# Kernel tuning notes

Hardware: AMD Instinct MI355X
Metric: run time of the kernel (lower is better)

Reference implementation:

```python
import jax, jax.numpy as jnp
import numpy as np

B = 8192
INPUT_DIM = 64   # history length / freq_dim
OUTPUT_DIM = 16
TEXT_DIM = 1024
TEXT_AIM = 128
H = 128          # lstm hidden_size (2 layers)


def _lin(key, out_d, in_d):
    k1, k2 = jax.random.split(key)
    s = 1.0 / np.sqrt(in_d)
    w = jax.random.uniform(k1, (out_d, in_d), jnp.float32, -s, s)
    b = jax.random.uniform(k2, (out_d,), jnp.float32, -s, s)
    return w, b


def setup_inputs() -> dict:
    key = jax.random.key(0)
    ks = jax.random.split(key, 16)
    inp = {}
    inp["data"] = jax.random.normal(ks[0], (B, INPUT_DIM), jnp.float32)
    inp["text_feature"] = jax.random.normal(ks[1], (B, TEXT_DIM), jnp.float32)
    # CrossAttention(text_aim_dim=128, freq_dim=input_dim=64)
    inp["q_w"], inp["q_b"] = _lin(ks[2], INPUT_DIM, INPUT_DIM)
    inp["k_w"], inp["k_b"] = _lin(ks[3], INPUT_DIM, TEXT_AIM)
    inp["v_w"], inp["v_b"] = _lin(ks[4], INPUT_DIM, TEXT_AIM)
    # text_proj: 1024 -> 256 -> 128
    inp["tp1_w"], inp["tp1_b"] = _lin(ks[5], 256, TEXT_DIM)
    inp["tp2_w"], inp["tp2_b"] = _lin(ks[6], TEXT_AIM, 256)
    # gate: 64 -> 128 -> 64
    inp["g1_w"], inp["g1_b"] = _lin(ks[7], 128, INPUT_DIM)
    inp["g2_w"], inp["g2_b"] = _lin(ks[8], INPUT_DIM, 128)
    # 2-layer LSTM, input size 1 (PyTorch i,f,g,o gate order)
    inp["w_ih0"], inp["b_ih0"] = _lin(ks[9], 4 * H, 1)
    inp["w_hh0"], inp["b_hh0"] = _lin(ks[10], 4 * H, H)
    inp["w_ih1"], inp["b_ih1"] = _lin(ks[11], 4 * H, H)
    inp["w_hh1"], inp["b_hh1"] = _lin(ks[12], 4 * H, H)
    # fc head: H -> H -> 1
    inp["fc1_w"], inp["fc1_b"] = _lin(ks[13], H, H)
    inp["fc2_w"], inp["fc2_b"] = _lin(ks[14], 1, H)
    return inp


def _cell(x, h, c, w_ih, w_hh, b_ih, b_hh):
    g = x @ w_ih.T + h @ w_hh.T + (b_ih + b_hh)
    i, f, gg, o = jnp.split(g, 4, axis=-1)
    c = jax.nn.sigmoid(f) * c + jax.nn.sigmoid(i) * jnp.tanh(gg)
    h = jax.nn.sigmoid(o) * jnp.tanh(c)
    return h, c


def _forward(data, text_feature, q_w, q_b, k_w, k_b, v_w, v_b,
             tp1_w, tp1_b, tp2_w, tp2_b, g1_w, g1_b, g2_w, g2_b,
             w_ih0, b_ih0, w_hh0, b_hh0, w_ih1, b_ih1, w_hh1, b_hh1,
             fc1_w, fc1_b, fc2_w, fc2_b):
    Bn = data.shape[0]
    z = jnp.zeros((Bn, H), data.dtype)
    # --- warmup pass over the full sequence (seq-major xs: (T, B, 1)) ---
    xs = data.T[:, :, None]

    def warm(carry, x_t):
        h0, c0, h1, c1 = carry
        h0, c0 = _cell(x_t, h0, c0, w_ih0, w_hh0, b_ih0, b_hh0)
        h1, c1 = _cell(h0, h1, c1, w_ih1, w_hh1, b_ih1, b_hh1)
        return (h0, c0, h1, c1), None

    (h0, c0, h1, c1), _ = jax.lax.scan(warm, (z, z, z, z), xs)

    def dec(carry, _):
        h0, c0, h1, c1, x_t = carry
        h0, c0 = _cell(x_t, h0, c0, w_ih0, w_hh0, b_ih0, b_hh0)
        h1, c1 = _cell(h0, h1, c1, w_ih1, w_hh1, b_ih1, b_hh1)
        hmid = jax.nn.leaky_relu(h1 @ fc1_w.T + fc1_b)
        pred = hmid @ fc2_w.T + fc2_b  # (B, 1)
        return (h0, c0, h1, c1, pred), pred

    (_, _, _, _, _), preds = jax.lax.scan(dec, (h0, c0, h1, c1, data[:, -1:]), None, length=OUTPUT_DIM)
    result = preds[:, :, 0].T  # (B, OUTPUT_DIM)

    # --- text-enhance branch: FFT features + cross-attention gating ---
    X = jnp.fft.rfft(data)                       # (B, 33)
    amp = jnp.abs(X)
    phase = jnp.angle(X)
    fftres = jnp.concatenate([amp, phase[:, 1:]], axis=1)  # (B, 65)
    dc, feat = fftres[:, :1], fftres[:, 1:]                # (B,1), (B,64)

    tp = jax.nn.leaky_relu(text_feature @ tp1_w.T + tp1_b) @ tp2_w.T + tp2_b  # (B, 128)
    Q = feat @ q_w.T + q_b
    K = tp @ k_w.T + k_b
    V = tp @ v_w.T + v_b
    adj = jax.nn.softmax(Q * K, axis=-1) * V  # (B, 64)

    gate = jax.nn.sigmoid(jax.nn.leaky_relu(adj @ g1_w.T + g1_b) @ g2_w.T + g2_b)  # (B, 64)

    full = jnp.concatenate([jnp.zeros_like(dc), adj], axis=1)  # (B, 65)
    n_freq = INPUT_DIM // 2
    amp2 = full[:, :n_freq + 1]                                 # (B, 33)
    ph2 = jnp.concatenate([jnp.zeros_like(dc), full[:, n_freq + 1:]], axis=1)  # (B, 33)
    Xr = jax.lax.complex(amp2 * jnp.cos(ph2), amp2 * jnp.sin(ph2))
    recon = jnp.fft.irfft(Xr, n=INPUT_DIM)  # (B, 64)

    g16 = gate[:, :OUTPUT_DIM]
    return g16 * result + (1.0 - g16) * recon[:, :OUTPUT_DIM]


def reference(data, text_feature, q_w, q_b, k_w, k_b, v_w, v_b,
              tp1_w, tp1_b, tp2_w, tp2_b, g1_w, g1_b, g2_w, g2_b,
              w_ih0, b_ih0, w_hh0, b_hh0, w_ih1, b_ih1, w_hh1, b_hh1,
              fc1_w, fc1_b, fc2_w, fc2_b):
    return _forward(data, text_feature, q_w, q_b, k_w, k_b, v_w, v_b,
                    tp1_w, tp1_b, tp2_w, tp2_b, g1_w, g1_b, g2_w, g2_b,
                    w_ih0, b_ih0, w_hh0, b_hh0, w_ih1, b_ih1, w_hh1, b_hh1,
                    fc1_w, fc1_b, fc2_w, fc2_b)
```

## Files before the change

### kernel.cpp

```cpp
#include <hip/hip_runtime.h>
#include <hip/hip_fp16.h>
#include <math.h>

typedef _Float16 half8 __attribute__((ext_vector_type(8)));
typedef float f32x4 __attribute__((ext_vector_type(4)));

#define W0F 0.09817477042468103f

#if __has_builtin(__builtin_amdgcn_exp2f)
#define EXP2F __builtin_amdgcn_exp2f
#else
#define EXP2F exp2f
#endif
#if __has_builtin(__builtin_amdgcn_rcpf)
#define RCPF __builtin_amdgcn_rcpf
#else
#define RCPF(x) (1.f/(x))
#endif

__device__ __forceinline__ float sigf(float x){
  return RCPF(1.f + EXP2F(-1.442695041f*x));
}
__device__ __forceinline__ float tanh_fast(float x){
  float t = EXP2F(2.885390082f*x);
  return 1.f - 2.f*RCPF(t + 1.f);
}
__device__ __forceinline__ float lrelu(float x){ return (x>0.f)? x : 0.01f*x; }

__device__ __forceinline__ uint32_t packhl(float x){
  __half h = __float2half(x);
  __half l = __float2half(x - __half2float(h));
  return (uint32_t)__half_as_ushort(h) | ((uint32_t)__half_as_ushort(l) << 16);
}

__device__ __forceinline__ void unpackA(const uint4 d0, const uint4 d1, half8& hi, half8& lo){
  union { half8 h; uint32_t u[4]; } H, L;
  H.u[0] = (d0.x & 0xffffu) | (d0.y << 16);
  H.u[1] = (d0.z & 0xffffu) | (d0.w << 16);
  H.u[2] = (d1.x & 0xffffu) | (d1.y << 16);
  H.u[3] = (d1.z & 0xffffu) | (d1.w << 16);
  L.u[0] = (d0.x >> 16) | (d0.y & 0xffff0000u);
  L.u[1] = (d0.z >> 16) | (d0.w & 0xffff0000u);
  L.u[2] = (d1.x >> 16) | (d1.y & 0xffff0000u);
  L.u[3] = (d1.z >> 16) | (d1.w & 0xffff0000u);
  hi = H.h; lo = L.h;
}

__device__ __forceinline__ f32x4 mfma2(half8 ah, half8 al, half8 bh, f32x4 c){
  c = __builtin_amdgcn_mfma_f32_16x16x32_f16(ah, bh, c, 0,0,0);
  c = __builtin_amdgcn_mfma_f32_16x16x32_f16(al, bh, c, 0,0,0);
  return c;
}

__global__ __launch_bounds__(256) void convert_w(
    const float* __restrict__ w_hh0, const float* __restrict__ w_ih1,
    const float* __restrict__ w_hh1, const float* __restrict__ fc1_w,
    const float* __restrict__ tp1_w, __half* __restrict__ wsH)
{
  int c = blockIdx.x*256 + threadIdx.x;
  const float* src; size_t dhi, dlo; int n, k, K;
  if (c < 24576){
    int m = c >> 13; int q = c & 8191;
    src = (m==0)? w_hh0 : ((m==1)? w_ih1 : w_hh1); K = 128;
    dhi = (size_t)m*131072 + (size_t)q*8; dlo = dhi + 65536;
    int tile = q >> 8, ks = (q >> 6) & 3, lane = q & 63;
    n = tile*16 + (lane & 15); k = ks*32 + (lane >> 4)*8;
  } else if (c < 26624){
    int q = c - 24576; src = fc1_w; K = 128;
    dhi = 393216 + (size_t)q*8; dlo = 409600 + (size_t)q*8;
    int tile = q >> 8, ks = (q >> 6) & 3, lane = q & 63;
    n = tile*16 + (lane & 15); k = ks*32 + (lane >> 4)*8;
  } else {
    int q = c - 26624; src = tp1_w; K = 1024;
    dhi = 425984 + (size_t)q*8; dlo = 688128 + (size_t)q*8;
    int tile = q >> 11, ks = (q >> 6) & 31, lane = q & 63;
    n = tile*16 + (lane & 15); k = ks*32 + (lane >> 4)*8;
  }
  float4 a = *(const float4*)(src + (size_t)n*K + k);
  float4 b = *(const float4*)(src + (size_t)n*K + k + 4);
  float vv[8] = {a.x,a.y,a.z,a.w,b.x,b.y,b.z,b.w};
  union { uint4 u; unsigned short s[8]; } HI, LO;
  #pragma unroll
  for (int j = 0; j < 8; ++j){
    __half hh = __float2half(vv[j]);
    __half ll = __float2half(vv[j] - __half2float(hh));
    HI.s[j] = __half_as_ushort(hh);
    LO.s[j] = __half_as_ushort(ll);
  }
  *(uint4*)(wsH + dhi) = HI.u;
  *(uint4*)(wsH + dlo) = LO.u;
}

__global__ __attribute__((amdgpu_flat_work_group_size(512,512), amdgpu_waves_per_eu(2,2)))
void mkty_main(
    const float* __restrict__ data, const float* __restrict__ text_feature,
    const float* __restrict__ q_w, const float* __restrict__ q_b,
    const float* __restrict__ k_w, const float* __restrict__ k_b,
    const float* __restrict__ v_w, const float* __restrict__ v_b,
    const float* __restrict__ tp1_b,
    const float* __restrict__ tp2_w, const float* __restrict__ tp2_b,
    const float* __restrict__ g1_w, const float* __restrict__ g1_b,
    const float* __restrict__ g2_w, const float* __restrict__ g2_b,
    const float* __restrict__ w_ih0, const float* __restrict__ b_ih0,
    const float* __restrict__ b_hh0,
    const float* __restrict__ b_ih1, const float* __restrict__ b_hh1,
    const float* __restrict__ fc1_b,
    const float* __restrict__ fc2_w, const float* __restrict__ fc2_b,
    const __half* __restrict__ wsH, float* __restrict__ out)
{
  __shared__ float s_x[32][64];
  __shared__ float s_gate[32][16];
  __shared__ float s_rec[32][16];
  __shared__ float s_res[32][16];
  __shared__ float s_pred[32];
  __shared__ float ctab[64], stab[64];
  __shared__ __align__(16) unsigned char POOL[84992];

  const int tid = threadIdx.x;
  const int w = tid >> 6, l = tid & 63;
  const int lm = l & 15, lq = l >> 4;
  const int s0blk = blockIdx.x * 32;

  { int s = tid >> 4, j = (tid*4) & 63;
    *(float4*)&s_x[s][j] = *(const float4*)(data + (size_t)(s0blk+s)*64 + j); }
  if (tid < 64){ float sv,cv; sincosf((float)tid*W0F,&sv,&cv);
    stab[tid] = (tid==32)?0.f:sv; ctab[tid]=cv; }
  __syncthreads();

  {
    float* h256 = (float*)POOL;
    uint32_t* tfp = (uint32_t*)(POOL + 33792);
    const half8* T1h = (const half8*)(wsH + 425984);
    const int t0 = 2*w;
    f32x4 acc[2][2];
    #pragma unroll
    for (int mt=0; mt<2; ++mt)
      #pragma unroll
      for (int nt=0; nt<2; ++nt){ f32x4 z = {0.f,0.f,0.f,0.f}; acc[mt][nt] = z; }
    for (int kc = 0; kc < 1024; kc += 64){
      __syncthreads();
      { int s = tid >> 4, j0 = (tid & 15)*4;
        float4 v = *(const float4*)(text_feature + (size_t)(s0blk+s)*1024 + kc + j0);
        uint4 p; p.x = packhl(v.x); p.y = packhl(v.y); p.z = packhl(v.z); p.w = packhl(v.w);
        *(uint4*)&tfp[s*68 + j0] = p; }
      __syncthreads();
      #pragma unroll
      for (int ks = 0; ks < 2; ++ks){
        half8 Ah[2], Al[2];
        #pragma unroll
        for (int mt = 0; mt < 2; ++mt){
          const uint32_t* pp = &tfp[(mt*16+lm)*68 + ks*32 + lq*8];
          unpackA(*(const uint4*)pp, *(const uint4*)(pp+4), Ah[mt], Al[mt]);
        }
        int ksg = (kc >> 5) + ks;
        #pragma unroll
        for (int nt = 0; nt < 2; ++nt){
          int ci = ((t0+nt)*32 + ksg)*64 + l;
          half8 bh = T1h[ci];
          #pragma unroll
          for (int mt = 0; mt < 2; ++mt)
            acc[mt][nt] = mfma2(Ah[mt],Al[mt],bh,acc[mt][nt]);
        }
      }
    }
    #pragma unroll
    for (int nt = 0; nt < 2; ++nt){
      int n = (t0+nt)*16 + lm;
      float bb = tp1_b[n];
      #pragma unroll
      for (int mt = 0; mt < 2; ++mt)
        #pragma unroll
        for (int r = 0; r < 4; ++r)
          h256[(mt*16 + lq*4 + r)*260 + n] = lrelu(acc[mt][nt][r] + bb);
    }
  }
  __syncthreads();

  {
    const float* h256 = (const float*)POOL;
    int o = tid & 127, soct = tid >> 7, ss = soct*8;
    float acc8[8];
    #pragma unroll
    for (int i=0;i<8;++i) acc8[i]=0.f;
    const float4* w2r = (const float4*)(tp2_w + o*256);
    #pragma unroll 4
    for (int k4 = 0; k4 < 64; ++k4){
      float4 w4 = w2r[k4];
      #pragma unroll
      for (int i = 0; i < 8; ++i){
        float4 hv = *(const float4*)&h256[(ss+i)*260 + k4*4];
        acc8[i] += w4.x*hv.x; acc8[i] += w4.y*hv.y;
        acc8[i] += w4.z*hv.z; acc8[i] += w4.w*hv.w;
      }
    }
    __syncthreads();
    float* tpT = (float*)(POOL + 33792);
    float bb = tp2_b[o];
    #pragma unroll
    for (int i=0;i<8;++i) tpT[(ss+i)*128 + o] = acc8[i] + bb;
  }
  __syncthreads();

  {
    float* featT = (float*)POOL;
    #pragma unroll
    for (int i = 0; i < 2; ++i){
      int task = tid + 512*i;
      int s = task >> 5;
      int k = (task & 31) + 1;
      float re = 0.f, im = 0.f;
      #pragma unroll 8
      for (int n = 0; n < 64; ++n){
        float d = s_x[s][n];
        int m = (k*n) & 63;
        re += d*ctab[m]; im -= d*stab[m];
      }
      if (k == 32) im = 0.f;
      featT[(k-1)*32 + s] = sqrtf(re*re + im*im);
      featT[(31+k)*32 + s] = atan2f(im, re);
    }
  }
  __syncthreads();

  {
    const float* featT = (const float*)POOL;
    const float* tpT = (const float*)(POOL + 33792);
    float* QK = (float*)(POOL + 8192);
    float* V  = (float*)(POOL + 16384);
    #pragma unroll
    for (int i = 0; i < 4; ++i){
      int task = tid + 512*i;
      int s = task >> 6, o = task & 63;
      float q = q_b[o];
      const float* qwr = q_w + o*64;
      #pragma unroll 4
      for (int k = 0; k < 64; ++k) q += qwr[k]*featT[k*32 + s];
      float kk = k_b[o], vv = v_b[o];
      const float* kwr = k_w + o*128;
      const float* vwr = v_w + o*128;
      const float* tps = tpT + s*128;
      #pragma unroll 4
      for (int k = 0; k < 128; ++k){ kk += kwr[k]*tps[k]; vv += vwr[k]*tps[k]; }
      QK[s*64+o] = q*kk; V[s*64+o] = vv;
    }
  }
  __syncthreads();

  if (tid < 32){
    float* QK = (float*)(POOL + 8192);
    const float* V = (const float*)(POOL + 16384);
    float mx = -1e30f;
    for (int o = 0; o < 64; ++o) mx = fmaxf(mx, QK[tid*64+o]);
    float sum = 0.f;
    for (int o = 0; o < 64; ++o){ float e = expf(QK[tid*64+o]-mx); QK[tid*64+o] = e; sum += e; }
    float inv = 1.f/sum;
    for (int o = 0; o < 64; ++o) QK[tid*64+o] *= inv*V[tid*64+o];
  }
  __syncthreads();

  {
    const float* ADJ = (const float*)(POOL + 8192);
    float* midT = (float*)(POOL + 33792);
    int j = tid & 127, soct = tid >> 7, ss = soct*8;
    float accm[8];
    float bb = g1_b[j];
    #pragma unroll
    for (int i=0;i<8;++i) accm[i]=bb;
    const float* wr = g1_w + j*64;
    #pragma unroll 4
    for (int k = 0; k < 64; ++k){
      float ww = wr[k];
      #pragma unroll
      for (int i=0;i<8;++i) accm[i] += ww*ADJ[(ss+i)*64 + k];
    }
    #pragma unroll
    for (int i=0;i<8;++i) midT[(ss+i)*128 + j] = lrelu(accm[i]);
  }
  __syncthreads();

  {
    int s = tid >> 4, o = tid & 15;
    const float* midT = (const float*)(POOL + 33792);
    const float* ADJ = (const float*)(POOL + 8192);
    float acc = g2_b[o];
    const float* wr = g2_w + o*128;
    #pragma unroll 4
    for (int k = 0; k < 128; ++k) acc += wr[k]*midT[s*128 + k];
    float gate = sigf(acc);
    float sum = 0.f;
    float a32 = ADJ[s*64+31], p32 = ADJ[s*64+63];
    #pragma unroll
    for (int k = 1; k < 32; ++k){
      float amp = ADJ[s*64 + k-1];
      float ph  = ADJ[s*64 + 31+k];
      int m = (k*o) & 63;
      sum += amp*cosf(ph + (float)m*W0F);
    }
    float parity = (o&1)? -1.f : 1.f;
    s_gate[s][o] = gate;
    s_rec[s][o] = (2.f*sum + parity*a32*cosf(p32))*(1.f/64.f);
  }
  __syncthreads();

  { uint32_t* hz = (uint32_t*)POOL;
    for (int i = tid; i < 13568; i += 512) hz[i] = 0; }
  if (tid < 32) s_pred[tid] = s_x[tid][63];

  const int u = 16*w + lm;
  float bias0[4], wx0[4], bias1[4];
  #pragma unroll
  for (int T = 0; T < 4; ++T){
    int n = T*128 + u;
    bias0[T] = b_ih0[n] + b_hh0[n];
    wx0[T]   = w_ih0[n];
    bias1[T] = b_ih1[n] + b_hh1[n];
  }
  const float fb = fc1_b[u];
  const float wcol = fc2_w[u];
  const float fb2 = fc2_b[0];
  const half8* WH0h = (const half8*)(wsH);
  const half8* WI1h = (const half8*)(wsH + 131072);
  const half8* WH1h = (const half8*)(wsH + 262144);
  const half8* F1h  = (const half8*)(wsH + 393216);
  __half* h0h = (__half*)(POOL);
  __half* h1h = (__half*)(POOL + 8704);
  float*  c0s = (float*)(POOL + 17408);
  float*  c1s = (float*)(POOL + 35840);
  float*  fc2p = (float*)(POOL + 54272);
  const int cbase = w*256 + l;

  half8 wh0[16], wi1[16], wh1[16];
  #pragma unroll
  for (int q = 0; q < 16; ++q){
    int nt = q >> 2, ks = q & 3;
    int ci = nt*2048 + ks*64 + cbase;
    wh0[q] = WH0h[ci];
    wi1[q] = WI1h[ci];
    wh1[q] = WH1h[ci];
  }
  #pragma unroll
  for (int q = 0; q < 16; ++q)
    asm volatile("" : "+v"(wh0[q]), "+v"(wi1[q]), "+v"(wh1[q]));
  __syncthreads();

  for (int t = 0; t < 80; ++t){
    float xv[2][4];
    #pragma unroll
    for (int mt = 0; mt < 2; ++mt)
      #pragma unroll
      for (int r = 0; r < 4; ++r){
        int m = mt*16 + lq*4 + r;
        xv[mt][r] = (t < 64) ? s_x[m][t] : s_pred[m];
      }
    f32x4 acc0[2][4];
    #pragma unroll
    for (int nt = 0; nt < 4; ++nt)
      #pragma unroll
      for (int mt = 0; mt < 2; ++mt){
        f32x4 a;
        #pragma unroll
        for (int r = 0; r < 4; ++r) a[r] = bias0[nt] + wx0[nt]*xv[mt][r];
        acc0[mt][nt] = a;
      }
    #pragma unroll
    for (int ks = 0; ks < 4; ++ks){
      half8 Ah[2];
      #pragma unroll
      for (int mt = 0; mt < 2; ++mt)
        Ah[mt] = *(const half8*)&h0h[(mt*16+lm)*136 + ks*32 + lq*8];
      #pragma unroll
      for (int nt = 0; nt < 4; ++nt)
        #pragma unroll
        for (int mt = 0; mt < 2; ++mt)
          acc0[mt][nt] = __builtin_amdgcn_mfma_f32_16x16x32_f16(Ah[mt], wh0[nt*4+ks], acc0[mt][nt], 0,0,0);
    }
    __syncthreads();
    #pragma unroll
    for (int mt = 0; mt < 2; ++mt)
      #pragma unroll
      for (int r = 0; r < 4; ++r){
        int cix = tid*9 + mt*4 + r;
        float gi = acc0[mt][0][r], gf = acc0[mt][1][r];
        float gg = acc0[mt][2][r], go = acc0[mt][3][r];
        float c = sigf(gf)*c0s[cix] + sigf(gi)*tanh_fast(gg);
        float h = sigf(go)*tanh_fast(c);
        c0s[cix] = c;
        h0h[(mt*16 + lq*4 + r)*136 + u] = __float2half(h);
      }
    __syncthreads();
    f32x4 acc1[2][4];
    #pragma unroll
    for (int nt = 0; nt < 4; ++nt)
      #pragma unroll
      for (int mt = 0; mt < 2; ++mt){
        f32x4 a; float bb = bias1[nt];
        a[0]=bb; a[1]=bb; a[2]=bb; a[3]=bb;
        acc1[mt][nt] = a;
      }
    #pragma unroll
    for (int ks = 0; ks < 4; ++ks){
      half8 Ah[2];
      #pragma unroll
      for (int mt = 0; mt < 2; ++mt)
        Ah[mt] = *(const half8*)&h0h[(mt*16+lm)*136 + ks*32 + lq*8];
      #pragma unroll
      for (int nt = 0; nt < 4; ++nt)
        #pragma unroll
        for (int mt = 0; mt < 2; ++mt)
          acc1[mt][nt] = __builtin_amdgcn_mfma_f32_16x16x32_f16(Ah[mt], wi1[nt*4+ks], acc1[mt][nt], 0,0,0);
    }
    #pragma unroll
    for (int ks = 0; ks < 4; ++ks){
      half8 Ah[2];
      #pragma unroll
      for (int mt = 0; mt < 2; ++mt)
        Ah[mt] = *(const half8*)&h1h[(mt*16+lm)*136 + ks*32 + lq*8];
      #pragma unroll
      for (int nt = 0; nt < 4; ++nt)
        #pragma unroll
        for (int mt = 0; mt < 2; ++mt)
          acc1[mt][nt] = __builtin_amdgcn_mfma_f32_16x16x32_f16(Ah[mt], wh1[nt*4+ks], acc1[mt][nt], 0,0,0);
    }
    __syncthreads();
    #pragma unroll
    for (int mt = 0; mt < 2; ++mt)
      #pragma unroll
      for (int r = 0; r < 4; ++r){
        int cix = tid*9 + mt*4 + r;
        float gi = acc1[mt][0][r], gf = acc1[mt][1][r];
        float gg = acc1[mt][2][r], go = acc1[mt][3][r];
        float c = sigf(gf)*c1s[cix] + sigf(gi)*tanh_fast(gg);
        float h = sigf(go)*tanh_fast(c);
        c1s[cix] = c;
        h1h[(mt*16 + lq*4 + r)*136 + u] = __float2half(h);
      }
    __syncthreads();

    if (t >= 64){
      f32x4 fa[2];
      #pragma unroll
      for (int mt = 0; mt < 2; ++mt){ f32x4 a; a[0]=fb;a[1]=fb;a[2]=fb;a[3]=fb; fa[mt]=a; }
      #pragma unroll
      for (int ks = 0; ks < 4; ++ks){
        half8 Ah[2];
        #pragma unroll
        for (int mt = 0; mt < 2; ++mt)
          Ah[mt] = *(const half8*)&h1h[(mt*16+lm)*136 + ks*32 + lq*8];
        int ci = (w*4 + ks)*64 + l;
        half8 bh = F1h[ci];
        #pragma unroll
        for (int mt = 0; mt < 2; ++mt)
          fa[mt] = __builtin_amdgcn_mfma_f32_16x16x32_f16(Ah[mt], bh, fa[mt], 0,0,0);
      }
      float pr[2][4];
      #pragma unroll
      for (int mt = 0; mt < 2; ++mt)
        #pragma unroll
        for (int r = 0; r < 4; ++r){
          float p = lrelu(fa[mt][r]) * wcol;
          p += __shfl_xor(p, 1, 16);
          p += __shfl_xor(p, 2, 16);
          p += __shfl_xor(p, 4, 16);
          p += __shfl_xor(p, 8, 16);
          pr[mt][r] = p;
        }
      if (lm == 0){
        #pragma unroll
        for (int mt = 0; mt < 2; ++mt)
          #pragma unroll
          for (int r = 0; r < 4; ++r)
            fc2p[(mt*16 + lq*4 + r)*8 + w] = pr[mt][r];
      }
      __syncthreads();
      if (tid < 32){
        float s = fb2;
        #pragma unroll
        for (int j = 0; j < 8; ++j) s += fc2p[tid*8 + j];
        s_pred[tid] = s;
        s_res[tid][t-64] = s;
      }
      __syncthreads();
    }
  }

  {
    int s = tid >> 4, d = tid & 15;
    float g = s_gate[s][d];
    out[(size_t)blockIdx.x*512 + tid] = g*s_res[s][d] + (1.f - g)*s_rec[s][d];
  }
}

extern "C" void kernel_launch(void* const* d_in, const int* in_sizes, int n_in,
                              void* d_out, int out_size, void* d_ws, size_t ws_size,
                              hipStream_t stream){
  const float* data =(const float*)d_in[0];
  const float* tf   =(const float*)d_in[1];
  const float* q_w  =(const float*)d_in[2];  const float* q_b  =(const float*)d_in[3];
  const float* k_w  =(const float*)d_in[4];  const float* k_b  =(const float*)d_in[5];
  const float* v_w  =(const float*)d_in[6];  const float* v_b  =(const float*)d_in[7];
  const float* tp1_w=(const float*)d_in[8];  const float* tp1_b=(const float*)d_in[9];
  const float* tp2_w=(const float*)d_in[10]; const float* tp2_b=(const float*)d_in[11];
  const float* g1_w =(const float*)d_in[12]; const float* g1_b =(const float*)d_in[13];
  const float* g2_w =(const float*)d_in[14]; const float* g2_b =(const float*)d_in[15];
  const float* w_ih0=(const float*)d_in[16]; const float* b_ih0=(const float*)d_in[17];
  const float* w_hh0=(const float*)d_in[18]; const float* b_hh0=(const float*)d_in[19];
  const float* w_ih1=(const float*)d_in[20]; const float* b_ih1=(const float*)d_in[21];
  const float* w_hh1=(const float*)d_in[22]; const float* b_hh1=(const float*)d_in[23];
  const float* fc1_w=(const float*)d_in[24]; const float* fc1_b=(const float*)d_in[25];
  const float* fc2_w=(const float*)d_in[26]; const float* fc2_b=(const float*)d_in[27];
  float* out=(float*)d_out;
  __half* wsH = (__half*)d_ws;

  convert_w<<<232,256,0,stream>>>(w_hh0, w_ih1, w_hh1, fc1_w, tp1_w, wsH);
  mkty_main<<<256,512,0,stream>>>(data, tf, q_w,q_b, k_w,k_b, v_w,v_b,
                                  tp1_b, tp2_w,tp2_b, g1_w,g1_b, g2_w,g2_b,
                                  w_ih0,b_ih0,b_hh0, b_ih1,b_hh1,
                                  fc1_b, fc2_w,fc2_b, wsH, out);
}
```

Measured before the change: 834.2 us.

## Double-buffer LSTM hidden states in LDS to drop two barriers per step

```diff
diff --git a/kernel.cpp b/kernel.cpp
--- a/kernel.cpp
+++ b/kernel.cpp
@@ -303,7 +303,7 @@
   __syncthreads();
 
   { uint32_t* hz = (uint32_t*)POOL;
-    for (int i = tid; i < 13568; i += 512) hz[i] = 0; }
+    for (int i = tid; i < 17920; i += 512) hz[i] = 0; }
   if (tid < 32) s_pred[tid] = s_x[tid][63];
 
   const int u = 16*w + lm;
@@ -322,28 +322,41 @@
   const half8* WI1h = (const half8*)(wsH + 131072);
   const half8* WH1h = (const half8*)(wsH + 262144);
   const half8* F1h  = (const half8*)(wsH + 393216);
-  __half* h0h = (__half*)(POOL);
-  __half* h1h = (__half*)(POOL + 8704);
-  float*  c0s = (float*)(POOL + 17408);
-  float*  c1s = (float*)(POOL + 35840);
-  float*  fc2p = (float*)(POOL + 54272);
+  __half* h0base = (__half*)(POOL);
+  __half* h1base = (__half*)(POOL + 17408);
+  float*  c0s = (float*)(POOL + 34816);
+  float*  c1s = (float*)(POOL + 53248);
+  float*  fc2p = (float*)(POOL + 71680);
   const int cbase = w*256 + l;
 
-  half8 wh0[16], wi1[16], wh1[16];
+  half8 wh0[16], wi1[16], wh1c[8];
   #pragma unroll
   for (int q = 0; q < 16; ++q){
     int nt = q >> 2, ks = q & 3;
     int ci = nt*2048 + ks*64 + cbase;
     wh0[q] = WH0h[ci];
     wi1[q] = WI1h[ci];
-    wh1[q] = WH1h[ci];
+  }
+  #pragma unroll
+  for (int q = 0; q < 8; ++q){
+    int nt = q >> 1, ks = q & 1;
+    wh1c[q] = WH1h[nt*2048 + ks*64 + cbase];
   }
   #pragma unroll
   for (int q = 0; q < 16; ++q)
-    asm volatile("" : "+v"(wh0[q]), "+v"(wi1[q]), "+v"(wh1[q]));
+    asm volatile("" : "+v"(wh0[q]), "+v"(wi1[q]));
+  #pragma unroll
+  for (int q = 0; q < 8; ++q)
+    asm volatile("" : "+v"(wh1c[q]));
   __syncthreads();
 
   for (int t = 0; t < 80; ++t){
+    const int cur = t & 1;
+    __half* h0r = h0base + cur*4352;
+    __half* h0w = h0base + (cur^1)*4352;
+    __half* h1r = h1base + cur*4352;
+    __half* h1w = h1base + (cur^1)*4352;
+
     float xv[2][4];
     #pragma unroll
     for (int mt = 0; mt < 2; ++mt)
@@ -367,14 +380,13 @@
       half8 Ah[2];
       #pragma unroll
       for (int mt = 0; mt < 2; ++mt)
-        Ah[mt] = *(const half8*)&h0h[(mt*16+lm)*136 + ks*32 + lq*8];
+        Ah[mt] = *(const half8*)&h0r[(mt*16+lm)*136 + ks*32 + lq*8];
       #pragma unroll
       for (int nt = 0; nt < 4; ++nt)
         #pragma unroll
         for (int mt = 0; mt < 2; ++mt)
           acc0[mt][nt] = __builtin_amdgcn_mfma_f32_16x16x32_f16(Ah[mt], wh0[nt*4+ks], acc0[mt][nt], 0,0,0);
     }
-    __syncthreads();
     #pragma unroll
     for (int mt = 0; mt < 2; ++mt)
       #pragma unroll
@@ -385,7 +397,7 @@
         float c = sigf(gf)*c0s[cix] + sigf(gi)*tanh_fast(gg);
         float h = sigf(go)*tanh_fast(c);
         c0s[cix] = c;
-        h0h[(mt*16 + lq*4 + r)*136 + u] = __float2half(h);
+        h0w[(mt*16 + lq*4 + r)*136 + u] = __float2half(h);
       }
     __syncthreads();
     f32x4 acc1[2][4];
@@ -402,7 +414,7 @@
       half8 Ah[2];
       #pragma unroll
       for (int mt = 0; mt < 2; ++mt)
-        Ah[mt] = *(const half8*)&h0h[(mt*16+lm)*136 + ks*32 + lq*8];
+        Ah[mt] = *(const half8*)&h0w[(mt*16+lm)*136 + ks*32 + lq*8];
       #pragma unroll
       for (int nt = 0; nt < 4; ++nt)
         #pragma unroll
@@ -410,18 +422,33 @@
           acc1[mt][nt] = __builtin_amdgcn_mfma_f32_16x16x32_f16(Ah[mt], wi1[nt*4+ks], acc1[mt][nt], 0,0,0);
     }
     #pragma unroll
-    for (int ks = 0; ks < 4; ++ks){
+    for (int ks = 0; ks < 2; ++ks){
       half8 Ah[2];
       #pragma unroll
       for (int mt = 0; mt < 2; ++mt)
-        Ah[mt] = *(const half8*)&h1h[(mt*16+lm)*136 + ks*32 + lq*8];
+        Ah[mt] = *(const half8*)&h1r[(mt*16+lm)*136 + ks*32 + lq*8];
       #pragma unroll
       for (int nt = 0; nt < 4; ++nt)
         #pragma unroll
         for (int mt = 0; mt < 2; ++mt)
-          acc1[mt][nt] = __builtin_amdgcn_mfma_f32_16x16x32_f16(Ah[mt], wh1[nt*4+ks], acc1[mt][nt], 0,0,0);
-    }
-    __syncthreads();
+          acc1[mt][nt] = __builtin_amdgcn_mfma_f32_16x16x32_f16(Ah[mt], wh1c[nt*2+ks], acc1[mt][nt], 0,0,0);
+    }
+    #pragma unroll
+    for (int ks = 2; ks < 4; ++ks){
+      half8 Bw[4];
+      #pragma unroll
+      for (int nt = 0; nt < 4; ++nt)
+        Bw[nt] = WH1h[nt*2048 + ks*64 + cbase];
+      half8 Ah[2];
+      #pragma unroll
+      for (int mt = 0; mt < 2; ++mt)
+        Ah[mt] = *(const half8*)&h1r[(mt*16+lm)*136 + ks*32 + lq*8];
+      #pragma unroll
+      for (int nt = 0; nt < 4; ++nt)
+        #pragma unroll
+        for (int mt = 0; mt < 2; ++mt)
+          acc1[mt][nt] = __builtin_amdgcn_mfma_f32_16x16x32_f16(Ah[mt], Bw[nt], acc1[mt][nt], 0,0,0);
+    }
     #pragma unroll
     for (int mt = 0; mt < 2; ++mt)
       #pragma unroll
@@ -432,7 +459,7 @@
         float c = sigf(gf)*c1s[cix] + sigf(gi)*tanh_fast(gg);
         float h = sigf(go)*tanh_fast(c);
         c1s[cix] = c;
-        h1h[(mt*16 + lq*4 + r)*136 + u] = __float2half(h);
+        h1w[(mt*16 + lq*4 + r)*136 + u] = __float2half(h);
       }
     __syncthreads();
 
@@ -445,7 +472,7 @@
         half8 Ah[2];
         #pragma unroll
         for (int mt = 0; mt < 2; ++mt)
-          Ah[mt] = *(const half8*)&h1h[(mt*16+lm)*136 + ks*32 + lq*8];
+          Ah[mt] = *(const half8*)&h1w[(mt*16+lm)*136 + ks*32 + lq*8];
         int ci = (w*4 + ks)*64 + l;
         half8 bh = F1h[ci];
         #pragma unroll
```

Result: slower. 976.3 us (+17.0%).
